# Kernel tuning notes

Hardware: AMD Instinct MI355X
Metric: run time of the kernel (lower is better)

The kernel has to match this reference:

```python
import jax, jax.numpy as jnp
import numpy as np

INF = 1e9  # large additive-mask constant (original code's INF)
D_KEY = 64


def setup_inputs() -> dict:
    key = jax.random.key(0)
    kq, kk, kv = jax.random.split(key, 3)
    B, S, D = 8, 2048, 64
    return {
        "query": jax.random.normal(kq, (B, S, D), dtype=jnp.float32),
        "key": jax.random.normal(kk, (B, S, D), dtype=jnp.float32),
        "value": jax.random.normal(kv, (B, S, D), dtype=jnp.float32),
    }


def reference(query, key, value):
    # scores: [B, Sq, Sk]
    scores = jnp.einsum("bqd,bkd->bqk", query, key)
    Sk = key.shape[1]
    # strict upper-triangular additive causal mask, subtracted BEFORE scaling
    tri = jnp.triu(jnp.ones((Sk, Sk), dtype=scores.dtype), k=1) * INF
    scores = scores - tri[None, :, :]
    scale = jnp.asarray(np.sqrt(D_KEY), dtype=scores.dtype)
    attn = jax.nn.softmax(scores / scale, axis=2)  # dropout ratio = 0.0
    return jnp.einsum("bqk,bkd->bqd", attn, value)
```

## Files before the change

### kernel.cpp

```cpp
#include <hip/hip_runtime.h>
#include <hip/hip_bf16.h>

typedef __attribute__((ext_vector_type(8))) short bf16x8;
typedef __attribute__((ext_vector_type(4))) float f32x4;
typedef __attribute__((ext_vector_type(4))) unsigned short us4;

#define BATCH 8
#define SEQ 2048
#define DIM 64
#define QB 64
#define NQT 32
#define NKT 32
#define TE 4096
#define CH 4
#define CPB 144
#define QSCALE (0.125f * 1.44269504088896f)
#define THR 8.0f

__device__ __forceinline__ unsigned short f2bf(float f) {
    return __builtin_bit_cast(unsigned short, __float2bfloat16(f));
}
__device__ __forceinline__ float bf2f(unsigned short u) {
    return __builtin_bit_cast(float, (unsigned)u << 16);
}

__device__ __forceinline__ int kswz(int row, int d) {
    return (row * DIM + d) ^ ((row & 7) << 3);
}
__device__ __forceinline__ int vswz(int d, int kv) {
    return (d * 64 + kv) ^ ((((d & 7) ^ ((d >> 2) & 7)) & 7) << 3);
}
__device__ __forceinline__ int pswz(int row, int kv) {
    return (row * 64 + kv) ^ ((row & 7) << 3);
}

#define GLOAD16(gsrc, ldst)                                                     \
    __builtin_amdgcn_global_load_lds(                                           \
        (const __attribute__((address_space(1))) void*)(gsrc),                  \
        (__attribute__((address_space(3))) void*)(ldst), 16, 0, 0)

__global__ __launch_bounds__(256) void prep_kernel(const float* __restrict__ K,
                                                   const float* __restrict__ V,
                                                   unsigned short* __restrict__ Kp,
                                                   unsigned short* __restrict__ Vp) {
    const int batch = blockIdx.x & 7;
    const int t = blockIdx.x >> 3;
    const int tile = batch * NKT + t;
    const int tid = threadIdx.x;
    const float* Kt = K + (size_t)tile * TE;
    const float* Vt = V + (size_t)tile * TE;
    unsigned short* Kd = Kp + (size_t)tile * TE;
    unsigned short* Vd = Vp + (size_t)tile * TE;
    #pragma unroll
    for (int i = 0; i < 4; ++i) {
        int idx = i * 256 + tid;
        int row = idx >> 4;
        int d0 = (idx & 15) << 2;
        f32x4 kf = *(const f32x4*)(Kt + row * DIM + d0);
        us4 kb = {f2bf(kf[0]), f2bf(kf[1]), f2bf(kf[2]), f2bf(kf[3])};
        *(us4*)(&Kd[kswz(row, d0)]) = kb;
    }
    const int dt4 = tid & 15, k4 = tid >> 4;
    f32x4 vf[4];
    #pragma unroll
    for (int rr = 0; rr < 4; ++rr)
        vf[rr] = *(const f32x4*)(Vt + (k4 * 4 + rr) * DIM + dt4 * 4);
    #pragma unroll
    for (int dd = 0; dd < 4; ++dd) {
        us4 vb = {f2bf(vf[0][dd]), f2bf(vf[1][dd]), f2bf(vf[2][dd]), f2bf(vf[3][dd])};
        *(us4*)(&Vd[vswz(dt4 * 4 + dd, k4 * 4)]) = vb;
    }
}

__global__ __launch_bounds__(256, 4) void fa_kernel(const float* __restrict__ Q,
                                                    const unsigned short* __restrict__ Kp,
                                                    const unsigned short* __restrict__ Vp,
                                                    unsigned short* __restrict__ PO,
                                                    float* __restrict__ PM,
                                                    float* __restrict__ PL,
                                                    float* __restrict__ O) {
    __shared__ unsigned short KL[2][4096];
    __shared__ unsigned short VL[2][4096];
    __shared__ unsigned short PB[4][1024];

    const int tid = threadIdx.x;
    const int w = tid >> 6, lane = tid & 63, g = lane >> 4, c = lane & 15;

    const int slot = blockIdx.x;
    const int batch = slot & 7;
    const int c0 = (CPB - 1) - (slot >> 3);
    int g2 = 0;
    #pragma unroll
    for (int gg = 1; gg < 8; ++gg) g2 = (c0 >= 2 * gg * (gg + 1)) ? gg : g2;
    const int nc = g2 + 1;
    const int x = c0 - 2 * g2 * nc;
    const int qrow = (x >= nc) + (x >= 2 * nc) + (x >= 3 * nc);
    const int sp = x - qrow * nc;
    const int qi = 4 * g2 + qrow;

    const int q0 = qi * QB;
    const int nt = qi + 1;
    const int t0 = sp * CH;
    const int t1 = (t0 + CH < nt) ? (t0 + CH) : nt;
    const int tiles = t1 - t0;
    const bool dchunk = (t1 == nt);

    const unsigned short* Kb = Kp + (size_t)batch * NKT * TE;
    const unsigned short* Vb = Vp + (size_t)batch * NKT * TE;

#define STAGE_TILE(tidx, buf)                                          \
    do {                                                               \
        const char* Ks_ = (const char*)(Kb + (size_t)(tidx) * TE);     \
        const char* Vs_ = (const char*)(Vb + (size_t)(tidx) * TE);     \
        char* kd_ = (char*)&KL[buf][0];                                \
        char* vd_ = (char*)&VL[buf][0];                                \
        _Pragma("unroll")                                              \
        for (int i_ = 0; i_ < 2; ++i_) {                               \
            int off_ = (w * 2 + i_) * 1024;                            \
            GLOAD16(Ks_ + off_ + lane * 16, kd_ + off_);               \
            GLOAD16(Vs_ + off_ + lane * 16, vd_ + off_);               \
        }                                                              \
    } while (0)

    STAGE_TILE(t0, 0);

    const float* Qrow = Q + (size_t)(batch * SEQ + q0 + w * 16 + c) * DIM;
    f32x4 qf0 = *(const f32x4*)(Qrow + g * 8);
    f32x4 qf1 = *(const f32x4*)(Qrow + g * 8 + 4);
    f32x4 qf2 = *(const f32x4*)(Qrow + 32 + g * 8);
    f32x4 qf3 = *(const f32x4*)(Qrow + 32 + g * 8 + 4);
    bf16x8 qa[2];
    #pragma unroll
    for (int j = 0; j < 4; ++j) {
        qa[0][j]     = (short)f2bf(qf0[j] * QSCALE);
        qa[0][j + 4] = (short)f2bf(qf1[j] * QSCALE);
        qa[1][j]     = (short)f2bf(qf2[j] * QSCALE);
        qa[1][j + 4] = (short)f2bf(qf3[j] * QSCALE);
    }

    float m[4], lsum[4];
    f32x4 o[4];
    #pragma unroll
    for (int r = 0; r < 4; ++r) { m[r] = -1e30f; lsum[r] = 0.f; }
    #pragma unroll
    for (int dt = 0; dt < 4; ++dt) o[dt] = f32x4{0.f, 0.f, 0.f, 0.f};

    __builtin_amdgcn_sched_barrier(0);
    asm volatile("s_waitcnt vmcnt(0)" ::: "memory");
    __builtin_amdgcn_s_barrier();
    __builtin_amdgcn_sched_barrier(0);

    for (int u = 0; u < tiles; ++u) {
        const int cb = u & 1;
        const bool last = (u == tiles - 1);

        if (!last) STAGE_TILE(t0 + u + 1, cb ^ 1);

        f32x4 s[4];
        #pragma unroll
        for (int n = 0; n < 4; ++n) s[n] = f32x4{0.f, 0.f, 0.f, 0.f};
        __builtin_amdgcn_s_setprio(1);
        #pragma unroll
        for (int n = 0; n < 4; ++n)
            #pragma unroll
            for (int f = 0; f < 2; ++f) {
                bf16x8 kb = *(bf16x8*)(&KL[cb][kswz(n * 16 + c, f * 32 + g * 8)]);
                s[n] = __builtin_amdgcn_mfma_f32_16x16x32_bf16(qa[f], kb, s[n], 0, 0, 0);
            }
        __builtin_amdgcn_s_setprio(0);

        if (dchunk && last) {
            const int dbase = (nt - 1) * 64;
            #pragma unroll
            for (int n = 0; n < 4; ++n) {
                int col = dbase + n * 16 + c;
                #pragma unroll
                for (int r = 0; r < 4; ++r)
                    if (col > q0 + w * 16 + g * 4 + r) s[n][r] = -1e30f;
            }
        }

        float pmx[4];
        #pragma unroll
        for (int r = 0; r < 4; ++r)
            pmx[r] = fmaxf(fmaxf(s[0][r], s[1][r]), fmaxf(s[2][r], s[3][r]));
        bool need = false;
        #pragma unroll
        for (int r = 0; r < 4; ++r) need |= (pmx[r] > m[r] + THR);
        if (__any(need)) {
            #pragma unroll
            for (int r = 0; r < 4; ++r) {
                float t2 = pmx[r];
                t2 = fmaxf(t2, __shfl_xor(t2, 1));
                t2 = fmaxf(t2, __shfl_xor(t2, 2));
                t2 = fmaxf(t2, __shfl_xor(t2, 4));
                t2 = fmaxf(t2, __shfl_xor(t2, 8));
                float mn = fmaxf(m[r], t2);
                float alpha = exp2f(m[r] - mn);
                m[r] = mn;
                lsum[r] *= alpha;
                #pragma unroll
                for (int dt = 0; dt < 4; ++dt) o[dt][r] *= alpha;
            }
        }
        #pragma unroll
        for (int n = 0; n < 4; ++n)
            #pragma unroll
            for (int r = 0; r < 4; ++r) {
                float pe = exp2f(s[n][r] - m[r]);
                s[n][r] = pe;
                lsum[r] += pe;
            }

        unsigned short* Pw = &PB[w][0];
        #pragma unroll
        for (int n = 0; n < 4; ++n)
            #pragma unroll
            for (int r = 0; r < 4; ++r)
                Pw[pswz(g * 4 + r, n * 16 + c)] = f2bf(s[n][r]);
        asm volatile("s_waitcnt lgkmcnt(0)" ::: "memory");
        __builtin_amdgcn_sched_barrier(0);

        __builtin_amdgcn_s_setprio(1);
        #pragma unroll
        for (int ks = 0; ks < 2; ++ks) {
            bf16x8 pa = *(bf16x8*)(&Pw[pswz(c, ks * 32 + g * 8)]);
            #pragma unroll
            for (int dt = 0; dt < 4; ++dt) {
                bf16x8 vb = *(bf16x8*)(&VL[cb][vswz(dt * 16 + c, ks * 32 + g * 8)]);
                o[dt] = __builtin_amdgcn_mfma_f32_16x16x32_bf16(pa, vb, o[dt], 0, 0, 0);
            }
        }
        __builtin_amdgcn_s_setprio(0);

        if (!last) {
            __builtin_amdgcn_sched_barrier(0);
            asm volatile("s_waitcnt vmcnt(0)" ::: "memory");
            __builtin_amdgcn_s_barrier();
            __builtin_amdgcn_sched_barrier(0);
        }
    }

    float l[4];
    #pragma unroll
    for (int r = 0; r < 4; ++r) {
        float ts = lsum[r];
        ts += __shfl_xor(ts, 1);
        ts += __shfl_xor(ts, 2);
        ts += __shfl_xor(ts, 4);
        ts += __shfl_xor(ts, 8);
        l[r] = ts;
    }

    if (nt <= CH) {
        #pragma unroll
        for (int r = 0; r < 4; ++r) {
            float inv = 1.f / l[r];
            float* Orow = O + (size_t)(batch * SEQ + q0 + w * 16 + g * 4 + r) * DIM;
            #pragma unroll
            for (int dt = 0; dt < 4; ++dt)
                Orow[dt * 16 + c] = o[dt][r] * inv;
        }
    } else {
        unsigned short* Pbase = PO + (size_t)slot * (QB * DIM);
        #pragma unroll
        for (int r = 0; r < 4; ++r) {
            int rowin = w * 16 + g * 4 + r;
            #pragma unroll
            for (int dt = 0; dt < 4; ++dt)
                Pbase[rowin * DIM + dt * 16 + c] = f2bf(o[dt][r]);
            if (c == 0) {
                PM[(size_t)slot * QB + rowin] = m[r];
                PL[(size_t)slot * QB + rowin] = l[r];
            }
        }
    }
#undef STAGE_TILE
}

__global__ __launch_bounds__(256) void combine_kernel(const unsigned short* __restrict__ PO,
                                                      const float* __restrict__ PM,
                                                      const float* __restrict__ PL,
                                                      float* __restrict__ O) {
    const int tid = threadIdx.x;
    const int ridx = blockIdx.x * 16 + (tid >> 4);
    const int d0 = (tid & 15) << 2;
    const int batch = ridx / 1792;
    const int rem = ridx - batch * 1792;
    const int qi = 4 + (rem >> 6);
    const int rowin = rem & 63;
    const int a = qi >> 2, b = qi & 3;
    const int nc = a + 1;
    const int pfx = (a + 1) * (2 * a + b);

    float mstar = -1e30f;
    #pragma unroll 4
    for (int sp = 0; sp < nc; ++sp) {
        int sl = ((CPB - 1 - (pfx + sp)) << 3) | batch;
        mstar = fmaxf(mstar, PM[(size_t)sl * QB + rowin]);
    }
    float ls = 0.f;
    f32x4 os = {0.f, 0.f, 0.f, 0.f};
    #pragma unroll 4
    for (int sp = 0; sp < nc; ++sp) {
        int sl = ((CPB - 1 - (pfx + sp)) << 3) | batch;
        float wgt = exp2f(PM[(size_t)sl * QB + rowin] - mstar);
        ls += PL[(size_t)sl * QB + rowin] * wgt;
        us4 po = *(const us4*)(PO + (size_t)sl * (QB * DIM) + rowin * DIM + d0);
        os[0] += bf2f(po[0]) * wgt;
        os[1] += bf2f(po[1]) * wgt;
        os[2] += bf2f(po[2]) * wgt;
        os[3] += bf2f(po[3]) * wgt;
    }
    const int grow = batch * SEQ + qi * 64 + rowin;
    float inv = 1.f / ls;
    f32x4 res = os * inv;
    *(f32x4*)(O + (size_t)grow * DIM + d0) = res;
}

extern "C" void kernel_launch(void* const* d_in, const int* in_sizes, int n_in,
                              void* d_out, int out_size, void* d_ws, size_t ws_size,
                              hipStream_t stream) {
    const float* Q = (const float*)d_in[0];
    const float* K = (const float*)d_in[1];
    const float* V = (const float*)d_in[2];
    float* O = (float*)d_out;
    (void)in_sizes; (void)n_in; (void)out_size; (void)ws_size;

    const size_t kvelems = (size_t)BATCH * SEQ * DIM;
    unsigned short* Kp = (unsigned short*)d_ws;
    unsigned short* Vp = Kp + kvelems;
    unsigned short* PO = Vp + kvelems;
    float* PM = (float*)(PO + (size_t)BATCH * CPB * QB * DIM);
    float* PL = PM + (size_t)BATCH * CPB * QB;

    prep_kernel<<<BATCH * NKT, 256, 0, stream>>>(K, V, Kp, Vp);
    fa_kernel<<<BATCH * CPB, 256, 0, stream>>>(Q, Kp, Vp, PO, PM, PL, O);
    combine_kernel<<<BATCH * 28 * 64 / 16, 256, 0, stream>>>(PO, PM, PL, O);
}
```

Measured before the change: 36.70 us.

## Halve KV tile to 32 keys to double occupancy of attention kernel

Changes the inner KV tile from 64 to 32 keys, halving the shared-memory footprint for K, V and P buffers and raising launch bounds to 8 blocks per CU. The V pre-transpose layout and swizzles are rewritten for 32-key sub-tiles, and the causal mask now covers the last two sub-tiles. Chunk coverage stays the same at 8 sub-tiles. The aim is more resident waves to hide latency, at the cost of twice as many loop iterations, barriers and softmax rescale checks per key.

Measured after the change: 40.06 us. 9.2% more time.

```diff
diff --git a/kernel.cpp b/kernel.cpp
--- a/kernel.cpp
+++ b/kernel.cpp
@@ -12,7 +12,8 @@
 #define NQT 32
 #define NKT 32
 #define TE 4096
-#define CH 4
+#define T32E 2048
+#define CH32 8
 #define CPB 144
 #define QSCALE (0.125f * 1.44269504088896f)
 #define THR 8.0f
@@ -27,11 +28,11 @@
 __device__ __forceinline__ int kswz(int row, int d) {
     return (row * DIM + d) ^ ((row & 7) << 3);
 }
-__device__ __forceinline__ int vswz(int d, int kv) {
-    return (d * 64 + kv) ^ ((((d & 7) ^ ((d >> 2) & 7)) & 7) << 3);
-}
-__device__ __forceinline__ int pswz(int row, int kv) {
-    return (row * 64 + kv) ^ ((row & 7) << 3);
+__device__ __forceinline__ int vswz32(int d, int kv) {
+    return d * 32 + (kv ^ ((((d & 7) ^ ((d >> 2) & 7)) & 3) << 3));
+}
+__device__ __forceinline__ int pswz32(int row, int kv) {
+    return row * 32 + (kv ^ ((row & 3) << 3));
 }
 
 #define GLOAD16(gsrc, ldst)                                                     \
@@ -61,27 +62,30 @@
         *(us4*)(&Kd[kswz(row, d0)]) = kb;
     }
     const int dt4 = tid & 15, k4 = tid >> 4;
+    const int t32 = k4 >> 3;
+    const int kvl = (k4 & 7) * 4;
     f32x4 vf[4];
     #pragma unroll
     for (int rr = 0; rr < 4; ++rr)
         vf[rr] = *(const f32x4*)(Vt + (k4 * 4 + rr) * DIM + dt4 * 4);
+    unsigned short* Vd32 = Vd + t32 * T32E;
     #pragma unroll
     for (int dd = 0; dd < 4; ++dd) {
         us4 vb = {f2bf(vf[0][dd]), f2bf(vf[1][dd]), f2bf(vf[2][dd]), f2bf(vf[3][dd])};
-        *(us4*)(&Vd[vswz(dt4 * 4 + dd, k4 * 4)]) = vb;
-    }
-}
-
-__global__ __launch_bounds__(256, 4) void fa_kernel(const float* __restrict__ Q,
+        *(us4*)(&Vd32[vswz32(dt4 * 4 + dd, kvl)]) = vb;
+    }
+}
+
+__global__ __launch_bounds__(256, 8) void fa_kernel(const float* __restrict__ Q,
                                                     const unsigned short* __restrict__ Kp,
                                                     const unsigned short* __restrict__ Vp,
                                                     unsigned short* __restrict__ PO,
                                                     float* __restrict__ PM,
                                                     float* __restrict__ PL,
                                                     float* __restrict__ O) {
-    __shared__ unsigned short KL[2][4096];
-    __shared__ unsigned short VL[2][4096];
-    __shared__ unsigned short PB[4][1024];
+    __shared__ unsigned short KL[2][2048];
+    __shared__ unsigned short VL[2][2048];
+    __shared__ unsigned short PB[4][512];
 
     const int tid = threadIdx.x;
     const int w = tid >> 6, lane = tid & 63, g = lane >> 4, c = lane & 15;
@@ -99,43 +103,40 @@
     const int qi = 4 * g2 + qrow;
 
     const int q0 = qi * QB;
-    const int nt = qi + 1;
-    const int t0 = sp * CH;
-    const int t1 = (t0 + CH < nt) ? (t0 + CH) : nt;
+    const int nt32 = 2 * qi + 2;
+    const int t0 = sp * CH32;
+    const int t1 = (t0 + CH32 < nt32) ? (t0 + CH32) : nt32;
     const int tiles = t1 - t0;
-    const bool dchunk = (t1 == nt);
+    const bool dchunk = (t1 == nt32);
 
     const unsigned short* Kb = Kp + (size_t)batch * NKT * TE;
     const unsigned short* Vb = Vp + (size_t)batch * NKT * TE;
 
-#define STAGE_TILE(tidx, buf)                                          \
+#define STAGE_TILE(t32idx, buf)                                        \
     do {                                                               \
-        const char* Ks_ = (const char*)(Kb + (size_t)(tidx) * TE);     \
-        const char* Vs_ = (const char*)(Vb + (size_t)(tidx) * TE);     \
-        char* kd_ = (char*)&KL[buf][0];                                \
-        char* vd_ = (char*)&VL[buf][0];                                \
-        _Pragma("unroll")                                              \
-        for (int i_ = 0; i_ < 2; ++i_) {                               \
-            int off_ = (w * 2 + i_) * 1024;                            \
-            GLOAD16(Ks_ + off_ + lane * 16, kd_ + off_);               \
-            GLOAD16(Vs_ + off_ + lane * 16, vd_ + off_);               \
-        }                                                              \
+        const char* Ks_ = (const char*)Kb + (size_t)(t32idx) * 4096;   \
+        const char* Vs_ = (const char*)Vb + (size_t)(t32idx) * 4096;   \
+        int off_ = w * 1024;                                           \
+        GLOAD16(Ks_ + off_ + lane * 16, (char*)&KL[buf][0] + off_);    \
+        GLOAD16(Vs_ + off_ + lane * 16, (char*)&VL[buf][0] + off_);    \
     } while (0)
 
     STAGE_TILE(t0, 0);
 
     const float* Qrow = Q + (size_t)(batch * SEQ + q0 + w * 16 + c) * DIM;
-    f32x4 qf0 = *(const f32x4*)(Qrow + g * 8);
-    f32x4 qf1 = *(const f32x4*)(Qrow + g * 8 + 4);
-    f32x4 qf2 = *(const f32x4*)(Qrow + 32 + g * 8);
-    f32x4 qf3 = *(const f32x4*)(Qrow + 32 + g * 8 + 4);
     bf16x8 qa[2];
-    #pragma unroll
-    for (int j = 0; j < 4; ++j) {
-        qa[0][j]     = (short)f2bf(qf0[j] * QSCALE);
-        qa[0][j + 4] = (short)f2bf(qf1[j] * QSCALE);
-        qa[1][j]     = (short)f2bf(qf2[j] * QSCALE);
-        qa[1][j + 4] = (short)f2bf(qf3[j] * QSCALE);
+    {
+        f32x4 qf0 = *(const f32x4*)(Qrow + g * 8);
+        f32x4 qf1 = *(const f32x4*)(Qrow + g * 8 + 4);
+        f32x4 qf2 = *(const f32x4*)(Qrow + 32 + g * 8);
+        f32x4 qf3 = *(const f32x4*)(Qrow + 32 + g * 8 + 4);
+        #pragma unroll
+        for (int j = 0; j < 4; ++j) {
+            qa[0][j]     = (short)f2bf(qf0[j] * QSCALE);
+            qa[0][j + 4] = (short)f2bf(qf1[j] * QSCALE);
+            qa[1][j]     = (short)f2bf(qf2[j] * QSCALE);
+            qa[1][j + 4] = (short)f2bf(qf3[j] * QSCALE);
+        }
     }
 
     float m[4], lsum[4];
@@ -156,12 +157,12 @@
 
         if (!last) STAGE_TILE(t0 + u + 1, cb ^ 1);
 
-        f32x4 s[4];
-        #pragma unroll
-        for (int n = 0; n < 4; ++n) s[n] = f32x4{0.f, 0.f, 0.f, 0.f};
+        f32x4 s[2];
+        #pragma unroll
+        for (int n = 0; n < 2; ++n) s[n] = f32x4{0.f, 0.f, 0.f, 0.f};
         __builtin_amdgcn_s_setprio(1);
         #pragma unroll
-        for (int n = 0; n < 4; ++n)
+        for (int n = 0; n < 2; ++n)
             #pragma unroll
             for (int f = 0; f < 2; ++f) {
                 bf16x8 kb = *(bf16x8*)(&KL[cb][kswz(n * 16 + c, f * 32 + g * 8)]);
@@ -169,10 +170,10 @@
             }
         __builtin_amdgcn_s_setprio(0);
 
-        if (dchunk && last) {
-            const int dbase = (nt - 1) * 64;
-            #pragma unroll
-            for (int n = 0; n < 4; ++n) {
+        if (dchunk && u >= tiles - 2) {
+            const int dbase = (t0 + u) * 32;
+            #pragma unroll
+            for (int n = 0; n < 2; ++n) {
                 int col = dbase + n * 16 + c;
                 #pragma unroll
                 for (int r = 0; r < 4; ++r)
@@ -183,7 +184,7 @@
         float pmx[4];
         #pragma unroll
         for (int r = 0; r < 4; ++r)
-            pmx[r] = fmaxf(fmaxf(s[0][r], s[1][r]), fmaxf(s[2][r], s[3][r]));
+            pmx[r] = fmaxf(s[0][r], s[1][r]);
         bool need = false;
         #pragma unroll
         for (int r = 0; r < 4; ++r) need |= (pmx[r] > m[r] + THR);
@@ -204,7 +205,7 @@
             }
         }
         #pragma unroll
-        for (int n = 0; n < 4; ++n)
+        for (int n = 0; n < 2; ++n)
             #pragma unroll
             for (int r = 0; r < 4; ++r) {
                 float pe = exp2f(s[n][r] - m[r]);
@@ -214,20 +215,19 @@
 
         unsigned short* Pw = &PB[w][0];
         #pragma unroll
-        for (int n = 0; n < 4; ++n)
+        for (int n = 0; n < 2; ++n)
             #pragma unroll
             for (int r = 0; r < 4; ++r)
-                Pw[pswz(g * 4 + r, n * 16 + c)] = f2bf(s[n][r]);
+                Pw[pswz32(g * 4 + r, n * 16 + c)] = f2bf(s[n][r]);
         asm volatile("s_waitcnt lgkmcnt(0)" ::: "memory");
         __builtin_amdgcn_sched_barrier(0);
 
         __builtin_amdgcn_s_setprio(1);
-        #pragma unroll
-        for (int ks = 0; ks < 2; ++ks) {
-            bf16x8 pa = *(bf16x8*)(&Pw[pswz(c, ks * 32 + g * 8)]);
+        {
+            bf16x8 pa = *(bf16x8*)(&Pw[pswz32(c, g * 8)]);
             #pragma unroll
             for (int dt = 0; dt < 4; ++dt) {
-                bf16x8 vb = *(bf16x8*)(&VL[cb][vswz(dt * 16 + c, ks * 32 + g * 8)]);
+                bf16x8 vb = *(bf16x8*)(&VL[cb][vswz32(dt * 16 + c, g * 8)]);
                 o[dt] = __builtin_amdgcn_mfma_f32_16x16x32_bf16(pa, vb, o[dt], 0, 0, 0);
             }
         }
@@ -252,7 +252,7 @@
         l[r] = ts;
     }
 
-    if (nt <= CH) {
+    if (nt32 <= CH32) {
         #pragma unroll
         for (int r = 0; r < 4; ++r) {
             float inv = 1.f / l[r];
```

## Halve KV split chunk size and rework slot mapping with online-max combine

Applied to the files above, without the earlier changes.

Reduces the KV tiles per split chunk from 4 to 2, so the grid grows from 144 to 272 chunks per batch. The slot-to-(query tile, split) decode is rewritten for the new pairing of query tiles. The combine kernel now merges partials in a single pass with a running max instead of two passes over PM. The aim is finer work units for better load balance across CUs, at the cost of more partial-result traffic and more combine work.

After: 41.16 us. 12.2% more time.

```diff
diff --git a/kernel.cpp b/kernel.cpp
--- a/kernel.cpp
+++ b/kernel.cpp
@@ -12,8 +12,8 @@
 #define NQT 32
 #define NKT 32
 #define TE 4096
-#define CH 4
-#define CPB 144
+#define CH 2
+#define CPB 272
 #define QSCALE (0.125f * 1.44269504088896f)
 #define THR 8.0f
 
@@ -89,14 +89,14 @@
     const int slot = blockIdx.x;
     const int batch = slot & 7;
     const int c0 = (CPB - 1) - (slot >> 3);
-    int g2 = 0;
-    #pragma unroll
-    for (int gg = 1; gg < 8; ++gg) g2 = (c0 >= 2 * gg * (gg + 1)) ? gg : g2;
-    const int nc = g2 + 1;
-    const int x = c0 - 2 * g2 * nc;
-    const int qrow = (x >= nc) + (x >= 2 * nc) + (x >= 3 * nc);
-    const int sp = x - qrow * nc;
-    const int qi = 4 * g2 + qrow;
+    int a = 0;
+    #pragma unroll
+    for (int gg = 1; gg < 16; ++gg) a = (c0 >= gg * (gg + 1)) ? gg : a;
+    const int nc = a + 1;
+    const int x = c0 - a * (a + 1);
+    int qi, sp;
+    if (x < nc) { qi = 2 * a; sp = x; }
+    else        { qi = 2 * a + 1; sp = x - nc; }
 
     const int q0 = qi * QB;
     const int nt = qi + 1;
@@ -252,7 +252,7 @@
         l[r] = ts;
     }
 
-    if (nt <= CH) {
+    if (nc == 1) {
         #pragma unroll
         for (int r = 0; r < 4; ++r) {
             float inv = 1.f / l[r];
@@ -285,26 +285,26 @@
     const int tid = threadIdx.x;
     const int ridx = blockIdx.x * 16 + (tid >> 4);
     const int d0 = (tid & 15) << 2;
-    const int batch = ridx / 1792;
-    const int rem = ridx - batch * 1792;
-    const int qi = 4 + (rem >> 6);
+    const int batch = ridx / 1920;
+    const int rem = ridx - batch * 1920;
+    const int qi = 2 + (rem >> 6);
     const int rowin = rem & 63;
-    const int a = qi >> 2, b = qi & 3;
+    const int a = qi >> 1, b = qi & 1;
     const int nc = a + 1;
-    const int pfx = (a + 1) * (2 * a + b);
-
-    float mstar = -1e30f;
-    #pragma unroll 4
+    const int pfx = (a + b) * (a + 1);
+
+    float mrun = -1e30f, ls = 0.f;
+    f32x4 os = {0.f, 0.f, 0.f, 0.f};
     for (int sp = 0; sp < nc; ++sp) {
         int sl = ((CPB - 1 - (pfx + sp)) << 3) | batch;
-        mstar = fmaxf(mstar, PM[(size_t)sl * QB + rowin]);
-    }
-    float ls = 0.f;
-    f32x4 os = {0.f, 0.f, 0.f, 0.f};
-    #pragma unroll 4
-    for (int sp = 0; sp < nc; ++sp) {
-        int sl = ((CPB - 1 - (pfx + sp)) << 3) | batch;
-        float wgt = exp2f(PM[(size_t)sl * QB + rowin] - mstar);
+        float mi = PM[(size_t)sl * QB + rowin];
+        if (mi > mrun) {
+            float sc = exp2f(mrun - mi);
+            ls *= sc;
+            os *= sc;
+            mrun = mi;
+        }
+        float wgt = exp2f(mi - mrun);
         ls += PL[(size_t)sl * QB + rowin] * wgt;
         us4 po = *(const us4*)(PO + (size_t)sl * (QB * DIM) + rowin * DIM + d0);
         os[0] += bf2f(po[0]) * wgt;
@@ -336,5 +336,5 @@
 
     prep_kernel<<<BATCH * NKT, 256, 0, stream>>>(K, V, Kp, Vp);
     fa_kernel<<<BATCH * CPB, 256, 0, stream>>>(Q, Kp, Vp, PO, PM, PL, O);
-    combine_kernel<<<BATCH * 28 * 64 / 16, 256, 0, stream>>>(PO, PM, PL, O);
-}
+    combine_kernel<<<BATCH * 30 * 64 / 16, 256, 0, stream>>>(PO, PM, PL, O);
+}
```
